# Kernel optimization log

Measured on AMD Instinct MI355X. Metric: run time of the kernel, lower is better.

Reference implementation:

```python
import jax, jax.numpy as jnp
import numpy as np

N = 100000
IN_DIM, HID_DIM, OUT_DIM = 256, 128, 128
DROPOUT_P = 0.1


def _gcn_conv(x, src, dst, W, b, n_nodes):
    # PyG GCNConv: x' = D^{-1/2} (A+I) D^{-1/2} (x W^T) + b
    # src/dst already include self-loops.
    h = x @ W.T  # (N, out)
    deg = jax.ops.segment_sum(jnp.ones_like(dst, dtype=h.dtype), dst,
                              num_segments=n_nodes)
    dinv = jnp.where(deg > 0, jax.lax.rsqrt(deg), 0.0)
    norm = dinv[src] * dinv[dst]                # (E+N,)
    msg = h[src] * norm[:, None]                # (E+N, out) - dominant traffic
    out = jax.ops.segment_sum(msg, dst, num_segments=n_nodes)
    return out + b


def setup_inputs() -> dict:
    key = jax.random.key(0)
    k1, k2, k3, k4, k5, k6 = jax.random.split(key, 6)
    X = jax.random.normal(k1, (N, IN_DIM), dtype=jnp.float32)
    edge_index = jax.random.randint(k2, (2, 1600000), 0, N, dtype=jnp.int64)
    # Glorot-ish init for linear weights (stored torch-style: (out, in))
    W1 = jax.random.normal(k3, (HID_DIM, IN_DIM), dtype=jnp.float32) / np.sqrt(IN_DIM)
    b1 = jnp.zeros((HID_DIM,), dtype=jnp.float32)
    W2 = jax.random.normal(k4, (OUT_DIM, HID_DIM), dtype=jnp.float32) / np.sqrt(HID_DIM)
    b2 = jnp.zeros((OUT_DIM,), dtype=jnp.float32)
    return {"X": X, "edge_index": edge_index, "W1": W1, "b1": b1,
            "W2": W2, "b2": b2}


def reference(X, edge_index, W1, b1, W2, b2):
    n = X.shape[0]
    loops = jnp.arange(n, dtype=edge_index.dtype)
    src = jnp.concatenate([edge_index[0], loops])
    dst = jnp.concatenate([edge_index[1], loops])

    h = _gcn_conv(X, src, dst, W1, b1, n)
    h = jax.nn.relu(h)
    # training-mode dropout with a fixed key (deterministic baseline)
    keep = jax.random.bernoulli(jax.random.key(42), 1.0 - DROPOUT_P, h.shape)
    h = jnp.where(keep, h / (1.0 - DROPOUT_P), 0.0)
    h = _gcn_conv(h, src, dst, W2, b2, n)
    return h
```

## Files before the change

kernel.cpp:

```cpp
#include <hip/hip_runtime.h>
#include <stdint.h>

#define IN_DIM 256
#define HID 128
#define BKT_BITS 6
#define BKT_SZ 64
#define MAXBKT 2048
#define NB_BLK 256

typedef __attribute__((ext_vector_type(8))) short short8v;
typedef __attribute__((ext_vector_type(4))) float f32x4;

__device__ __forceinline__ unsigned short f2bf(float f) {
    unsigned u = __float_as_uint(f);
    unsigned rnd = 0x7FFFu + ((u >> 16) & 1u);
    return (unsigned short)((u + rnd) >> 16);
}
__device__ __forceinline__ float bflo(unsigned v) { return __uint_as_float(v << 16); }
__device__ __forceinline__ float bfhi(unsigned v) { return __uint_as_float(v & 0xFFFF0000u); }

__device__ __forceinline__ unsigned rotl32(unsigned x, int r) {
    return (x << r) | (x >> (32 - r));
}
__device__ __forceinline__ float dropout_scale(unsigned idx) {
    const unsigned ks0 = 0u, ks1 = 42u, ks2 = 0x1BD11BF0u;
    unsigned x0 = 0u + ks0;
    unsigned x1 = idx + ks1;
#define TF_ROUND(r) { x0 += x1; x1 = rotl32(x1, r); x1 ^= x0; }
    TF_ROUND(13) TF_ROUND(15) TF_ROUND(26) TF_ROUND(6)
    x0 += ks1; x1 += ks2 + 1u;
    TF_ROUND(17) TF_ROUND(29) TF_ROUND(16) TF_ROUND(24)
    x0 += ks2; x1 += ks0 + 2u;
    TF_ROUND(13) TF_ROUND(15) TF_ROUND(26) TF_ROUND(6)
    x0 += ks0; x1 += ks1 + 3u;
    TF_ROUND(17) TF_ROUND(29) TF_ROUND(16) TF_ROUND(24)
    x0 += ks1; x1 += ks2 + 4u;
    TF_ROUND(13) TF_ROUND(15) TF_ROUND(26) TF_ROUND(6)
    x0 += ks2; x1 += ks0 + 5u;
#undef TF_ROUND
    unsigned bits = x0 ^ x1;
    float u = __uint_as_float(0x3F800000u | (bits >> 9)) - 1.0f;
    return (u < 0.9f) ? (1.0f / 0.9f) : 0.0f;
}

__global__ __launch_bounds__(256) void part_count(const int* __restrict__ dst,
                                                  int* __restrict__ counts,
                                                  int E, int nbkt, int per) {
    __shared__ int lh[MAXBKT];
    for (int i = threadIdx.x; i < nbkt; i += 256) lh[i] = 0;
    __syncthreads();
    int blk = blockIdx.x;
    int beg = blk * per, end = min(E, beg + per);
    for (int i = beg + threadIdx.x; i < end; i += 256)
        atomicAdd(&lh[dst[i] >> BKT_BITS], 1);
    __syncthreads();
    for (int b = threadIdx.x; b < nbkt; b += 256)
        counts[b * NB_BLK + blk] = lh[b];
}

__global__ __launch_bounds__(256) void scan2_local(const int* __restrict__ in,
                                                   int* __restrict__ out,
                                                   int* __restrict__ bsum, int M) {
    __shared__ int lds[256];
    int t = threadIdx.x;
    int base = blockIdx.x * 2048 + t * 8;
    int x[8], v[8];
    if (base + 7 < M) {
        int4 a = *(const int4*)(in + base);
        int4 b = *(const int4*)(in + base + 4);
        x[0] = a.x; x[1] = a.y; x[2] = a.z; x[3] = a.w;
        x[4] = b.x; x[5] = b.y; x[6] = b.z; x[7] = b.w;
    } else {
        for (int j = 0; j < 8; ++j) x[j] = (base + j < M) ? in[base + j] : 0;
    }
    int s = 0;
    for (int j = 0; j < 8; ++j) { v[j] = s; s += x[j]; }
    lds[t] = s;
    __syncthreads();
    for (int d = 1; d < 256; d <<= 1) {
        int val = lds[t];
        int add = (t >= d) ? lds[t - d] : 0;
        __syncthreads();
        lds[t] = val + add;
        __syncthreads();
    }
    int excl = lds[t] - s;
    for (int j = 0; j < 8; ++j)
        if (base + j < M) out[base + j] = excl + v[j];
    if (t == 255) bsum[blockIdx.x] = lds[255];
}
__global__ __launch_bounds__(256) void scan2_bsums(int* __restrict__ bsum, int nb) {
    __shared__ int lds[256];
    int t = threadIdx.x;
    int orig = (t < nb) ? bsum[t] : 0;
    lds[t] = orig;
    __syncthreads();
    for (int d = 1; d < 256; d <<= 1) {
        int val = lds[t];
        int add = (t >= d) ? lds[t - d] : 0;
        __syncthreads();
        lds[t] = val + add;
        __syncthreads();
    }
    if (t < nb) bsum[t] = lds[t] - orig;
}
__global__ void scan2_add(int* __restrict__ out, const int* __restrict__ bsum, int M) {
    int i = blockIdx.x * blockDim.x + threadIdx.x;
    if (i < M) out[i] += bsum[i >> 11];
}

__global__ __launch_bounds__(256) void part_scatter(const int* __restrict__ src,
                                                    const int* __restrict__ dst,
                                                    const int* __restrict__ cbase,
                                                    unsigned* __restrict__ packed,
                                                    int E, int nbkt, int per) {
    __shared__ int cur[MAXBKT];
    int blk = blockIdx.x;
    for (int b = threadIdx.x; b < nbkt; b += 256)
        cur[b] = cbase[b * NB_BLK + blk];
    __syncthreads();
    int beg = blk * per, end = min(E, beg + per);
    for (int i = beg + threadIdx.x; i < end; i += 256) {
        int d = dst[i];
        int pos = atomicAdd(&cur[d >> BKT_BITS], 1);
        packed[pos] = ((unsigned)src[i] << BKT_BITS) | (unsigned)(d & (BKT_SZ - 1));
    }
}

__global__ void extract_bbase(const int* __restrict__ cbase, int* __restrict__ bbase,
                              int nbkt, int E) {
    int b = blockIdx.x * blockDim.x + threadIdx.x;
    if (b < nbkt) bbase[b] = cbase[b * NB_BLK];
    if (b == nbkt) bbase[nbkt] = E;
}

__global__ __launch_bounds__(256) void bucket_finalize(const unsigned* __restrict__ packed,
                                                       const int* __restrict__ bbase,
                                                       int* __restrict__ ssrc,
                                                       int* __restrict__ offs,
                                                       float* __restrict__ dinv, int N) {
    __shared__ int hist[BKT_SZ];
    __shared__ int cur[BKT_SZ];
    int b = blockIdx.x;
    int t = threadIdx.x;
    int beg = bbase[b], end = bbase[b + 1];
    if (t < BKT_SZ) hist[t] = 0;
    __syncthreads();
    for (int i = beg + t; i < end; i += 256)
        atomicAdd(&hist[packed[i] & (BKT_SZ - 1)], 1);
    __syncthreads();
    if (t < BKT_SZ) cur[t] = hist[t];
    __syncthreads();
    for (int d = 1; d < BKT_SZ; d <<= 1) {
        int val = 0;
        if (t < BKT_SZ) { val = cur[t]; if (t >= d) val += cur[t - d]; }
        __syncthreads();
        if (t < BKT_SZ) cur[t] = val;
        __syncthreads();
    }
    if (t < BKT_SZ) {
        int node = b * BKT_SZ + t;
        int excl = cur[t] - hist[t];
        if (node < N) {
            offs[node] = beg + excl;
            dinv[node] = rsqrtf((float)(hist[t] + 1));
        }
        cur[t] = excl;
    }
    __syncthreads();
    for (int i = beg + t; i < end; i += 256) {
        unsigned p = packed[i];
        int dl = (int)(p & (BKT_SZ - 1));
        int pos = atomicAdd(&cur[dl], 1);
        ssrc[beg + pos] = (int)(p >> BKT_BITS);
    }
}

__global__ void cvt_w(const float* __restrict__ W, unsigned short* __restrict__ Wb, int n) {
    int i = blockIdx.x * blockDim.x + threadIdx.x;
    if (i < n) Wb[i] = f2bf(W[i]);
}

#define WP 264
#define AP 40
template <int A_BF16>
__global__ __launch_bounds__(256) void gemm_mfma(const void* __restrict__ Ap,
                                                 const unsigned short* __restrict__ Wb,
                                                 unsigned short* __restrict__ C,
                                                 int M, int K) {
    __shared__ unsigned short Wlds[128 * WP];
    __shared__ unsigned short Alds[64 * AP];
    const int t = threadIdx.x;
    const int bm = blockIdx.x * 64;

    const int kc = K >> 3;
    for (int c = t; c < 128 * kc; c += 256) {
        int row = c / kc, ko = c % kc;
        short8v w = *(const short8v*)(Wb + (size_t)row * K + ko * 8);
        *(short8v*)(&Wlds[row * WP + ko * 8]) = w;
    }

    const int w = t >> 6, l = t & 63;
    const int lr = l & 15, lk = l >> 4;
    const int sr = t >> 2, sc = t & 3;

    f32x4 acc[8] = {};

    for (int kb = 0; kb < K; kb += 32) {
        if (A_BF16) {
            short8v v = {};
            if (bm + sr < M)
                v = *(const short8v*)((const unsigned short*)Ap + (size_t)(bm + sr) * K + kb + sc * 8);
            *(short8v*)(&Alds[sr * AP + sc * 8]) = v;
        } else {
            short8v u = {};
            if (bm + sr < M) {
                const float* arow = (const float*)Ap + (size_t)(bm + sr) * K + kb + sc * 8;
                float4 f0 = *(const float4*)(arow);
                float4 f1 = *(const float4*)(arow + 4);
                u[0] = (short)f2bf(f0.x); u[1] = (short)f2bf(f0.y);
                u[2] = (short)f2bf(f0.z); u[3] = (short)f2bf(f0.w);
                u[4] = (short)f2bf(f1.x); u[5] = (short)f2bf(f1.y);
                u[6] = (short)f2bf(f1.z); u[7] = (short)f2bf(f1.w);
            }
            *(short8v*)(&Alds[sr * AP + sc * 8]) = u;
        }
        __syncthreads();

        short8v a = *(const short8v*)(&Alds[(w * 16 + lr) * AP + lk * 8]);
#pragma unroll
        for (int cb = 0; cb < 8; ++cb) {
            short8v b = *(const short8v*)(&Wlds[(cb * 16 + lr) * WP + kb + lk * 8]);
            acc[cb] = __builtin_amdgcn_mfma_f32_16x16x32_bf16(a, b, acc[cb], 0, 0, 0);
        }
        __syncthreads();
    }

#pragma unroll
    for (int cb = 0; cb < 8; ++cb) {
#pragma unroll
        for (int j = 0; j < 4; ++j) {
            int row = bm + w * 16 + lk * 4 + j;
            int col = cb * 16 + lr;
            if (row < M) C[(size_t)row * 128 + col] = f2bf(acc[cb][j]);
        }
    }
}

template <int MODE>
__global__ __launch_bounds__(256) void aggregate_csr(const unsigned* __restrict__ h,
                                                     const int* __restrict__ soff,
                                                     const int* __restrict__ ssrc,
                                                     const float* __restrict__ dinv,
                                                     const float* __restrict__ bias,
                                                     void* __restrict__ outp,
                                                     int N, int E) {
    int n = blockIdx.x * 4 + (threadIdx.x >> 6);
    if (n >= N) return;
    const int lane = threadIdx.x & 63;
    const int g = lane >> 4;
    const int f0 = lane & 15;
    int start = soff[n];
    int end = (n + 1 < N) ? soff[n + 1] : E;
    float dn = dinv[n];

    float a0 = 0.f, a1 = 0.f, a2 = 0.f, a3 = 0.f,
          a4 = 0.f, a5 = 0.f, a6 = 0.f, a7 = 0.f;

    for (int i = start; i < end; i += 4) {
        int ig = i + g;
        int s = n;
        float wgt = 0.f;
        if (ig < end) { s = ssrc[ig]; wgt = dinv[s]; }
        uint4 v = *(const uint4*)(h + (size_t)s * 64 + f0 * 4);
        a0 = fmaf(wgt, bflo(v.x), a0);
        a1 = fmaf(wgt, bfhi(v.x), a1);
        a2 = fmaf(wgt, bflo(v.y), a2);
        a3 = fmaf(wgt, bfhi(v.y), a3);
        a4 = fmaf(wgt, bflo(v.z), a4);
        a5 = fmaf(wgt, bfhi(v.z), a5);
        a6 = fmaf(wgt, bflo(v.w), a6);
        a7 = fmaf(wgt, bfhi(v.w), a7);
    }

    a0 += __shfl_xor(a0, 16, 64); a0 += __shfl_xor(a0, 32, 64);
    a1 += __shfl_xor(a1, 16, 64); a1 += __shfl_xor(a1, 32, 64);
    a2 += __shfl_xor(a2, 16, 64); a2 += __shfl_xor(a2, 32, 64);
    a3 += __shfl_xor(a3, 16, 64); a3 += __shfl_xor(a3, 32, 64);
    a4 += __shfl_xor(a4, 16, 64); a4 += __shfl_xor(a4, 32, 64);
    a5 += __shfl_xor(a5, 16, 64); a5 += __shfl_xor(a5, 32, 64);
    a6 += __shfl_xor(a6, 16, 64); a6 += __shfl_xor(a6, 32, 64);
    a7 += __shfl_xor(a7, 16, 64); a7 += __shfl_xor(a7, 32, 64);

    uint4 hv = *(const uint4*)(h + (size_t)n * 64 + f0 * 4);
    unsigned hvg = (g == 0) ? hv.x : (g == 1) ? hv.y : (g == 2) ? hv.z : hv.w;
    float sx, sy;
    if (g == 0)      { sx = a0; sy = a1; }
    else if (g == 1) { sx = a2; sy = a3; }
    else if (g == 2) { sx = a4; sy = a5; }
    else             { sx = a6; sy = a7; }

    float ax = (sx + dn * bflo(hvg)) * dn;
    float ay = (sy + dn * bfhi(hvg)) * dn;
    float2 bv = ((const float2*)bias)[f0 * 4 + g];
    ax += bv.x;
    ay += bv.y;
    int fi = f0 * 8 + g * 2;
    if (MODE == 1) {
        unsigned idx = (unsigned)n * 128u + (unsigned)fi;
        ax = fmaxf(ax, 0.f) * dropout_scale(idx);
        ay = fmaxf(ay, 0.f) * dropout_scale(idx + 1u);
        ((unsigned*)outp)[(size_t)n * 64 + f0 * 4 + g] =
            (unsigned)f2bf(ax) | ((unsigned)f2bf(ay) << 16);
    } else {
        ((float2*)outp)[(size_t)n * 64 + f0 * 4 + g] = make_float2(ax, ay);
    }
}

extern "C" void kernel_launch(void* const* d_in, const int* in_sizes, int n_in,
                              void* d_out, int out_size, void* d_ws, size_t ws_size,
                              hipStream_t stream) {
    const float* X  = (const float*)d_in[0];
    const int*   ei = (const int*)d_in[1];
    const float* W1 = (const float*)d_in[2];
    const float* b1 = (const float*)d_in[3];
    const float* W2 = (const float*)d_in[4];
    const float* b2 = (const float*)d_in[5];
    float* out = (float*)d_out;

    const int N = in_sizes[0] / IN_DIM;
    const int E = in_sizes[1] / 2;
    const int* src = ei;
    const int* dst = ei + E;
    const int total = N * HID;
    const size_t N4 = (size_t)N * 4;
    const size_t tot2 = (size_t)total * 2;
    const int NBKT = (N + BKT_SZ - 1) >> BKT_BITS;
    const int M = NBKT * NB_BLK;
    const int per = (E + NB_BLK - 1) / NB_BLK;
    const int snb = (M + 2047) / 2048;

    char* ws = (char*)d_ws;
    size_t off = 0;
    unsigned short* hA = (unsigned short*)(ws + off); off += tot2;
    unsigned short* hB = (unsigned short*)(ws + off); off += tot2;
    float* dinv = (float*)(ws + off); off += N4;
    int* offs   = (int*)(ws + off); off += N4;
    int* counts = (int*)(ws + off); off += (size_t)M * 4;
    int* cbase  = (int*)(ws + off); off += (size_t)M * 4;
    int* bsum   = (int*)(ws + off); off += 4096;
    int* bbase  = (int*)(ws + off); off += (size_t)(MAXBKT + 1) * 4;
    unsigned* packed = (unsigned*)(ws + off); off += (size_t)E * 4;
    int* ssrc   = (int*)(ws + off); off += (size_t)E * 4;
    unsigned short* Wb1 = (unsigned short*)(ws + off); off += (size_t)HID * IN_DIM * 2;
    unsigned short* Wb2 = (unsigned short*)(ws + off);

    cvt_w<<<(HID * IN_DIM + 255) / 256, 256, 0, stream>>>(W1, Wb1, HID * IN_DIM);
    cvt_w<<<(HID * HID + 255) / 256, 256, 0, stream>>>(W2, Wb2, HID * HID);
    part_count<<<NB_BLK, 256, 0, stream>>>(dst, counts, E, NBKT, per);
    scan2_local<<<snb, 256, 0, stream>>>(counts, cbase, bsum, M);
    scan2_bsums<<<1, 256, 0, stream>>>(bsum, snb);
    scan2_add<<<(M + 255) / 256, 256, 0, stream>>>(cbase, bsum, M);
    part_scatter<<<NB_BLK, 256, 0, stream>>>(src, dst, cbase, packed, E, NBKT, per);
    extract_bbase<<<(NBKT + 256) / 256, 256, 0, stream>>>(cbase, bbase, NBKT, E);
    bucket_finalize<<<NBKT, 256, 0, stream>>>(packed, bbase, ssrc, offs, dinv, N);

    gemm_mfma<0><<<(N + 63) / 64, 256, 0, stream>>>(X, Wb1, hA, N, IN_DIM);
    aggregate_csr<1><<<(N + 3) / 4, 256, 0, stream>>>((const unsigned*)hA, offs, ssrc,
                                                      dinv, b1, hB, N, E);
    gemm_mfma<1><<<(N + 63) / 64, 256, 0, stream>>>(hB, Wb2, hA, N, HID);
    aggregate_csr<2><<<(N + 3) / 4, 256, 0, stream>>>((const unsigned*)hA, offs, ssrc,
                                                      dinv, b2, out, N, E);
}
```

Baseline: 301.7 us.

## Prescale GEMM output by dinv and unroll aggregation with zero-row padding

The GEMM epilogue now multiplies each output row by dinv[row], so the aggregation no longer has to load dinv[src] per edge and can sum neighbour rows directly. Out-of-range lanes point at a zeroed padding row (index N) instead of being predicated, and the gather loop is unrolled to two edges per group for more loads in flight. This removes a dependent random load per edge. In exchange, bf16 rounding now happens after the scaling, and a memset plus extra workspace are needed for the pad row.

```diff
diff --git a/kernel.cpp b/kernel.cpp
--- a/kernel.cpp
+++ b/kernel.cpp
@@ -186,6 +186,7 @@
 template <int A_BF16>
 __global__ __launch_bounds__(256) void gemm_mfma(const void* __restrict__ Ap,
                                                  const unsigned short* __restrict__ Wb,
+                                                 const float* __restrict__ scale,
                                                  unsigned short* __restrict__ C,
                                                  int M, int K) {
     __shared__ unsigned short Wlds[128 * WP];
@@ -236,13 +237,19 @@
         __syncthreads();
     }
 
+    float scv[4];
+#pragma unroll
+    for (int j = 0; j < 4; ++j) {
+        int row = bm + w * 16 + lk * 4 + j;
+        scv[j] = (row < M) ? scale[row] : 0.f;
+    }
 #pragma unroll
     for (int cb = 0; cb < 8; ++cb) {
 #pragma unroll
         for (int j = 0; j < 4; ++j) {
             int row = bm + w * 16 + lk * 4 + j;
             int col = cb * 16 + lr;
-            if (row < M) C[(size_t)row * 128 + col] = f2bf(acc[cb][j]);
+            if (row < M) C[(size_t)row * 128 + col] = f2bf(acc[cb][j] * scv[j]);
         }
     }
 }
@@ -267,20 +274,20 @@
     float a0 = 0.f, a1 = 0.f, a2 = 0.f, a3 = 0.f,
           a4 = 0.f, a5 = 0.f, a6 = 0.f, a7 = 0.f;
 
-    for (int i = start; i < end; i += 4) {
-        int ig = i + g;
-        int s = n;
-        float wgt = 0.f;
-        if (ig < end) { s = ssrc[ig]; wgt = dinv[s]; }
-        uint4 v = *(const uint4*)(h + (size_t)s * 64 + f0 * 4);
-        a0 = fmaf(wgt, bflo(v.x), a0);
-        a1 = fmaf(wgt, bfhi(v.x), a1);
-        a2 = fmaf(wgt, bflo(v.y), a2);
-        a3 = fmaf(wgt, bfhi(v.y), a3);
-        a4 = fmaf(wgt, bflo(v.z), a4);
-        a5 = fmaf(wgt, bfhi(v.z), a5);
-        a6 = fmaf(wgt, bflo(v.w), a6);
-        a7 = fmaf(wgt, bfhi(v.w), a7);
+    for (int i = start; i < end; i += 8) {
+        int i0 = i + g, i1 = i + g + 4;
+        int s0 = (i0 < end) ? ssrc[i0] : N;
+        int s1 = (i1 < end) ? ssrc[i1] : N;
+        uint4 v0 = *(const uint4*)(h + (size_t)s0 * 64 + f0 * 4);
+        uint4 v1 = *(const uint4*)(h + (size_t)s1 * 64 + f0 * 4);
+        a0 += bflo(v0.x); a1 += bfhi(v0.x);
+        a2 += bflo(v0.y); a3 += bfhi(v0.y);
+        a4 += bflo(v0.z); a5 += bfhi(v0.z);
+        a6 += bflo(v0.w); a7 += bfhi(v0.w);
+        a0 += bflo(v1.x); a1 += bfhi(v1.x);
+        a2 += bflo(v1.y); a3 += bfhi(v1.y);
+        a4 += bflo(v1.z); a5 += bfhi(v1.z);
+        a6 += bflo(v1.w); a7 += bfhi(v1.w);
     }
 
     a0 += __shfl_xor(a0, 16, 64); a0 += __shfl_xor(a0, 32, 64);
@@ -300,8 +307,8 @@
     else if (g == 2) { sx = a4; sy = a5; }
     else             { sx = a6; sy = a7; }
 
-    float ax = (sx + dn * bflo(hvg)) * dn;
-    float ay = (sy + dn * bfhi(hvg)) * dn;
+    float ax = (sx + bflo(hvg)) * dn;
+    float ay = (sy + bfhi(hvg)) * dn;
     float2 bv = ((const float2*)bias)[f0 * 4 + g];
     ax += bv.x;
     ay += bv.y;
@@ -342,7 +349,7 @@
 
     char* ws = (char*)d_ws;
     size_t off = 0;
-    unsigned short* hA = (unsigned short*)(ws + off); off += tot2;
+    unsigned short* hA = (unsigned short*)(ws + off); off += tot2 + HID * 2;
     unsigned short* hB = (unsigned short*)(ws + off); off += tot2;
     float* dinv = (float*)(ws + off); off += N4;
     int* offs   = (int*)(ws + off); off += N4;
@@ -355,6 +362,8 @@
     unsigned short* Wb1 = (unsigned short*)(ws + off); off += (size_t)HID * IN_DIM * 2;
     unsigned short* Wb2 = (unsigned short*)(ws + off);
 
+    hipMemsetAsync(hA + (size_t)N * HID, 0, HID * 2, stream);
+
     cvt_w<<<(HID * IN_DIM + 255) / 256, 256, 0, stream>>>(W1, Wb1, HID * IN_DIM);
     cvt_w<<<(HID * HID + 255) / 256, 256, 0, stream>>>(W2, Wb2, HID * HID);
     part_count<<<NB_BLK, 256, 0, stream>>>(dst, counts, E, NBKT, per);
@@ -365,10 +374,10 @@
     extract_bbase<<<(NBKT + 256) / 256, 256, 0, stream>>>(cbase, bbase, NBKT, E);
     bucket_finalize<<<NBKT, 256, 0, stream>>>(packed, bbase, ssrc, offs, dinv, N);
 
-    gemm_mfma<0><<<(N + 63) / 64, 256, 0, stream>>>(X, Wb1, hA, N, IN_DIM);
+    gemm_mfma<0><<<(N + 63) / 64, 256, 0, stream>>>(X, Wb1, dinv, hA, N, IN_DIM);
     aggregate_csr<1><<<(N + 3) / 4, 256, 0, stream>>>((const unsigned*)hA, offs, ssrc,
                                                       dinv, b1, hB, N, E);
-    gemm_mfma<1><<<(N + 63) / 64, 256, 0, stream>>>(hB, Wb2, hA, N, HID);
+    gemm_mfma<1><<<(N + 63) / 64, 256, 0, stream>>>(hB, Wb2, dinv, hA, N, HID);
     aggregate_csr<2><<<(N + 3) / 4, 256, 0, stream>>>((const unsigned*)hA, offs, ssrc,
                                                       dinv, b2, out, N, E);
 }
```

After: 307.3 us. About the same (+1.9%).
